# Performance work log

Hardware: AMD Instinct MI355X
Metric: run time of the kernel (lower is better)

The kernel has to match this reference:

```python
import jax, jax.numpy as jnp
import numpy as np

N_MOL = 100000   # molecules in batch
N_ATOMS = 40     # atoms per molecule
R = 2            # resonance representations per molecule


def setup_inputs() -> dict:
    key = jax.random.key(0)
    k1, k2, k3 = jax.random.split(key, 3)
    N = N_MOL * N_ATOMS * R  # flattened atom rows (8M)
    electronegativity = jax.random.normal(k1, (N,), dtype=jnp.float32)
    # hardness must be positive / away from zero (it is inverted)
    hardness = jax.random.uniform(k2, (N,), dtype=jnp.float32, minval=0.5, maxval=1.5)
    formal_charge = jax.random.randint(k3, (N,), -1, 2).astype(jnp.float32)
    idx = jnp.arange(N, dtype=jnp.int32)
    # layout: [mol0 rep0 (40 atoms), mol0 rep1 (40 atoms), mol1 rep0, ...]
    rep_seg = idx // N_ATOMS                       # molecule-representation segment id
    mol = idx // (N_ATOMS * R)
    j = idx % N_ATOMS                              # atom index within molecule
    out_idx = mol * N_ATOMS + j                    # output row for mean over reps
    return {
        "electronegativity": electronegativity,
        "hardness": hardness,
        "formal_charge": formal_charge,
        "rep_seg": rep_seg,
        "out_idx": out_idx,
        "num_segments": N_MOL * R,
        "num_out": N_MOL * N_ATOMS,
        "n_reps": R,
    }


def reference(electronegativity, hardness, formal_charge, rep_seg, out_idx,
              num_segments, num_out, n_reps):
    # Charge equalization (Gilson et al.) per molecule-representation segment s:
    #   inv_h_i = 1/h_i
    #   q_i = inv_h_i * ((dot(inv_h, e) + Q_s) / sum(inv_h) - e_i)
    inv_h = 1.0 / hardness
    A = jax.ops.segment_sum(inv_h, rep_seg, num_segments)                      # sum(1/h)
    B = jax.ops.segment_sum(inv_h * electronegativity, rep_seg, num_segments)  # dot(1/h, e)
    Q = jax.ops.segment_sum(formal_charge, rep_seg, num_segments)              # total charge
    lam = (B + Q) / A                                                          # Lagrange multiplier per segment
    q = inv_h * (lam[rep_seg] - electronegativity)                             # per-atom charge per rep
    # mean over the n_reps representations of each molecule (torch .mean(dim=0) + vstack)
    out = jax.ops.segment_sum(q, out_idx, num_out) / n_reps
    return out.reshape(-1, 1)
```

## Files before the change

kernel.cpp:

```cpp
#include <hip/hip_runtime.h>


typedef float f32x4 __attribute__((ext_vector_type(4)));

#define BLOCK 320
#define MPB   32
#define SEGS  (MPB * 2)

__global__ __launch_bounds__(BLOCK) void cpc_kernel(
    const float* __restrict__ elneg,
    const float* __restrict__ hard,
    const float* __restrict__ fchg,
    float* __restrict__ out,
    int n_mol)
{
    __shared__ float s_pa[SEGS * 11];
    __shared__ float s_pb[SEGS * 11];
    __shared__ float s_pq[SEGS * 11];
    __shared__ float s_lam[SEGS];

    const int t = threadIdx.x;
    const int m = t / 10;
    const int s = t - m * 10;
    const long long mol_base = (long long)blockIdx.x * MPB;
    const int lm = min(MPB, (int)(n_mol - mol_base));
    const bool act = (m < lm);

    const long long g0 = (mol_base + m) * 80 + 4 * s;

    f32x4 h0, e0, f0, h1, e1, f1;
    h0.x=1;h0.y=1;h0.z=1;h0.w=1; h1=h0;
    e0.x=0;e0.y=0;e0.z=0;e0.w=0; e1=e0; f0=e0; f1=e0;
    if (act) {
        h0 = __builtin_nontemporal_load((const f32x4*)(hard  + g0));
        h1 = __builtin_nontemporal_load((const f32x4*)(hard  + g0 + 40));
        e0 = __builtin_nontemporal_load((const f32x4*)(elneg + g0));
        e1 = __builtin_nontemporal_load((const f32x4*)(elneg + g0 + 40));
        f0 = __builtin_nontemporal_load((const f32x4*)(fchg  + g0));
        f1 = __builtin_nontemporal_load((const f32x4*)(fchg  + g0 + 40));
    }

    f32x4 i0, i1;
    i0.x = 1.0f / h0.x; i0.y = 1.0f / h0.y; i0.z = 1.0f / h0.z; i0.w = 1.0f / h0.w;
    i1.x = 1.0f / h1.x; i1.y = 1.0f / h1.y; i1.z = 1.0f / h1.z; i1.w = 1.0f / h1.w;

    if (act) {
        const int b0 = (2 * m)     * 11 + s;
        const int b1 = (2 * m + 1) * 11 + s;
        s_pa[b0] = (i0.x + i0.y) + (i0.z + i0.w);
        s_pb[b0] = (i0.x * e0.x + i0.y * e0.y) + (i0.z * e0.z + i0.w * e0.w);
        s_pq[b0] = (f0.x + f0.y) + (f0.z + f0.w);
        s_pa[b1] = (i1.x + i1.y) + (i1.z + i1.w);
        s_pb[b1] = (i1.x * e1.x + i1.y * e1.y) + (i1.z * e1.z + i1.w * e1.w);
        s_pq[b1] = (f1.x + f1.y) + (f1.z + f1.w);
    }
    __syncthreads();

    if (t < 2 * lm) {
        float A = 0.f, B = 0.f, Q = 0.f;
        #pragma unroll
        for (int k = 0; k < 10; ++k) {
            A += s_pa[t * 11 + k];
            B += s_pb[t * 11 + k];
            Q += s_pq[t * 11 + k];
        }
        s_lam[t] = (B + Q) / A;
    }
    __syncthreads();

    if (act) {
        const float lam0 = s_lam[2 * m];
        const float lam1 = s_lam[2 * m + 1];
        f32x4 o;
        o.x = 0.5f * (i0.x * (lam0 - e0.x) + i1.x * (lam1 - e1.x));
        o.y = 0.5f * (i0.y * (lam0 - e0.y) + i1.y * (lam1 - e1.y));
        o.z = 0.5f * (i0.z * (lam0 - e0.z) + i1.z * (lam1 - e1.z));
        o.w = 0.5f * (i0.w * (lam0 - e0.w) + i1.w * (lam1 - e1.w));
        __builtin_nontemporal_store(o, (f32x4*)(out + (mol_base + m) * 40 + 4 * s));
    }
}

extern "C" void kernel_launch(void* const* d_in, const int* in_sizes, int n_in,
                              void* d_out, int out_size, void* d_ws, size_t ws_size,
                              hipStream_t stream) {
    const float* elneg = (const float*)d_in[0];
    const float* hard  = (const float*)d_in[1];
    const float* fchg  = (const float*)d_in[2];
    float* out = (float*)d_out;

    const int n_mol = out_size / 40;
    const int grid  = (n_mol + MPB - 1) / MPB;
    cpc_kernel<<<grid, BLOCK, 0, stream>>>(elneg, hard, fchg, out, n_mol);
}
```

Measured before the change: 23.93 us.

## Process two chunks per block with prefetch and double-buffered LDS reduction

Each block now handles two 16-molecule chunks. The next chunk's loads are issued before the barrier of the current one, and LDS buffers are double-buffered. Each thread loads one contiguous float4 per array rather than two strided ones, and the per-segment reduction reads vectorized f32x4 partials. Reciprocals use the fast rcp intrinsic, nontemporal loads and stores are dropped, and a launch-bounds occupancy hint is added. This adds LDS traffic for passing the rep-1 values and leaves half the threads idle in the output phase.

```diff
diff --git a/kernel.cpp b/kernel.cpp
--- a/kernel.cpp
+++ b/kernel.cpp
@@ -4,79 +4,103 @@
 typedef float f32x4 __attribute__((ext_vector_type(4)));
 
 #define BLOCK 320
-#define MPB   32
+#define MPB   16
 #define SEGS  (MPB * 2)
+#define PROW  3
 
-__global__ __launch_bounds__(BLOCK) void cpc_kernel(
+static __device__ __forceinline__ float hsum(f32x4 v) {
+    return (v.x + v.y) + (v.z + v.w);
+}
+
+__global__ __launch_bounds__(BLOCK, 8) void cpc_kernel(
     const float* __restrict__ elneg,
     const float* __restrict__ hard,
     const float* __restrict__ fchg,
     float* __restrict__ out,
-    int n_mol)
+    int n_mol, int nchunks)
 {
-    __shared__ float s_pa[SEGS * 11];
-    __shared__ float s_pb[SEGS * 11];
-    __shared__ float s_pq[SEGS * 11];
-    __shared__ float s_lam[SEGS];
+    __shared__ f32x4 s_pa [2][SEGS * PROW];
+    __shared__ f32x4 s_pbq[2][SEGS * PROW];
+    __shared__ f32x4 s_i1 [2][MPB * 10];
+    __shared__ f32x4 s_e1 [2][MPB * 10];
 
-    const int t = threadIdx.x;
-    const int m = t / 10;
-    const int s = t - m * 10;
-    const long long mol_base = (long long)blockIdx.x * MPB;
-    const int lm = min(MPB, (int)(n_mol - mol_base));
-    const bool act = (m < lm);
+    const int t  = threadIdx.x;
+    const int m  = t / 20;
+    const int s2 = t % 20;
+    const int r  = s2 / 10;
+    const int s  = s2 % 10;
 
-    const long long g0 = (mol_base + m) * 80 + 4 * s;
-
-    f32x4 h0, e0, f0, h1, e1, f1;
-    h0.x=1;h0.y=1;h0.z=1;h0.w=1; h1=h0;
-    e0.x=0;e0.y=0;e0.z=0;e0.w=0; e1=e0; f0=e0; f1=e0;
-    if (act) {
-        h0 = __builtin_nontemporal_load((const f32x4*)(hard  + g0));
-        h1 = __builtin_nontemporal_load((const f32x4*)(hard  + g0 + 40));
-        e0 = __builtin_nontemporal_load((const f32x4*)(elneg + g0));
-        e1 = __builtin_nontemporal_load((const f32x4*)(elneg + g0 + 40));
-        f0 = __builtin_nontemporal_load((const f32x4*)(fchg  + g0));
-        f1 = __builtin_nontemporal_load((const f32x4*)(fchg  + g0 + 40));
+    if (t < SEGS) {
+        ((float*)s_pa [0])[t*12+10] = 0.f; ((float*)s_pa [0])[t*12+11] = 0.f;
+        ((float*)s_pa [1])[t*12+10] = 0.f; ((float*)s_pa [1])[t*12+11] = 0.f;
+        ((float*)s_pbq[0])[t*12+10] = 0.f; ((float*)s_pbq[0])[t*12+11] = 0.f;
+        ((float*)s_pbq[1])[t*12+10] = 0.f; ((float*)s_pbq[1])[t*12+11] = 0.f;
     }
 
-    f32x4 i0, i1;
-    i0.x = 1.0f / h0.x; i0.y = 1.0f / h0.y; i0.z = 1.0f / h0.z; i0.w = 1.0f / h0.w;
-    i1.x = 1.0f / h1.x; i1.y = 1.0f / h1.y; i1.z = 1.0f / h1.z; i1.w = 1.0f / h1.w;
+    int c = blockIdx.x * 2;
+    bool act = (c < nchunks) && (c * MPB + m < n_mol);
+    f32x4 hv = {1,1,1,1}, ev = {0,0,0,0}, fv = {0,0,0,0};
+    if (act) {
+        const long long g = (long long)c * (MPB * 80) + 4 * t;
+        hv = *(const f32x4*)(hard  + g);
+        ev = *(const f32x4*)(elneg + g);
+        fv = *(const f32x4*)(fchg  + g);
+    }
 
-    if (act) {
-        const int b0 = (2 * m)     * 11 + s;
-        const int b1 = (2 * m + 1) * 11 + s;
-        s_pa[b0] = (i0.x + i0.y) + (i0.z + i0.w);
-        s_pb[b0] = (i0.x * e0.x + i0.y * e0.y) + (i0.z * e0.z + i0.w * e0.w);
-        s_pq[b0] = (f0.x + f0.y) + (f0.z + f0.w);
-        s_pa[b1] = (i1.x + i1.y) + (i1.z + i1.w);
-        s_pb[b1] = (i1.x * e1.x + i1.y * e1.y) + (i1.z * e1.z + i1.w * e1.w);
-        s_pq[b1] = (f1.x + f1.y) + (f1.z + f1.w);
-    }
-    __syncthreads();
+    int buf = 0;
+    #pragma unroll
+    for (int it = 0; it < 2; ++it) {
+        if (c >= nchunks) break;
 
-    if (t < 2 * lm) {
-        float A = 0.f, B = 0.f, Q = 0.f;
-        #pragma unroll
-        for (int k = 0; k < 10; ++k) {
-            A += s_pa[t * 11 + k];
-            B += s_pb[t * 11 + k];
-            Q += s_pq[t * 11 + k];
+        f32x4 iv;
+        iv.x = __builtin_amdgcn_rcpf(hv.x);
+        iv.y = __builtin_amdgcn_rcpf(hv.y);
+        iv.z = __builtin_amdgcn_rcpf(hv.z);
+        iv.w = __builtin_amdgcn_rcpf(hv.w);
+        const float pa  = hsum(iv);
+        const float pbq = ((iv.x*ev.x + iv.y*ev.y) + (iv.z*ev.z + iv.w*ev.w)) + hsum(fv);
+        if (act) {
+            const int seg = m * 2 + r;
+            ((float*)s_pa [buf])[seg*12 + s] = pa;
+            ((float*)s_pbq[buf])[seg*12 + s] = pbq;
+            if (r) { s_i1[buf][m*10 + s] = iv; s_e1[buf][m*10 + s] = ev; }
         }
-        s_lam[t] = (B + Q) / A;
-    }
-    __syncthreads();
+        const f32x4 i0 = iv, e0 = ev;
+        const int  cc = c;
+        const bool act_cur = act;
 
-    if (act) {
-        const float lam0 = s_lam[2 * m];
-        const float lam1 = s_lam[2 * m + 1];
-        f32x4 o;
-        o.x = 0.5f * (i0.x * (lam0 - e0.x) + i1.x * (lam1 - e1.x));
-        o.y = 0.5f * (i0.y * (lam0 - e0.y) + i1.y * (lam1 - e1.y));
-        o.z = 0.5f * (i0.z * (lam0 - e0.z) + i1.z * (lam1 - e1.z));
-        o.w = 0.5f * (i0.w * (lam0 - e0.w) + i1.w * (lam1 - e1.w));
-        __builtin_nontemporal_store(o, (f32x4*)(out + (mol_base + m) * 40 + 4 * s));
+        c += 1;
+        if (it == 0) {
+            act = (c < nchunks) && (c * MPB + m < n_mol);
+            if (act) {
+                const long long g = (long long)c * (MPB * 80) + 4 * t;
+                hv = *(const f32x4*)(hard  + g);
+                ev = *(const f32x4*)(elneg + g);
+                fv = *(const f32x4*)(fchg  + g);
+            }
+        }
+
+        __syncthreads();
+
+        if (r == 0 && act_cur) {
+            const int row0 = (m*2)     * PROW;
+            const int row1 = (m*2 + 1) * PROW;
+            const float A0 = hsum(s_pa [buf][row0]) + hsum(s_pa [buf][row0+1]) + hsum(s_pa [buf][row0+2]);
+            const float B0 = hsum(s_pbq[buf][row0]) + hsum(s_pbq[buf][row0+1]) + hsum(s_pbq[buf][row0+2]);
+            const float A1 = hsum(s_pa [buf][row1]) + hsum(s_pa [buf][row1+1]) + hsum(s_pa [buf][row1+2]);
+            const float B1 = hsum(s_pbq[buf][row1]) + hsum(s_pbq[buf][row1+1]) + hsum(s_pbq[buf][row1+2]);
+            const float lam0 = B0 / A0;
+            const float lam1 = B1 / A1;
+            const f32x4 i1 = s_i1[buf][m*10 + s];
+            const f32x4 e1 = s_e1[buf][m*10 + s];
+            f32x4 o;
+            o.x = 0.5f * (i0.x * (lam0 - e0.x) + i1.x * (lam1 - e1.x));
+            o.y = 0.5f * (i0.y * (lam0 - e0.y) + i1.y * (lam1 - e1.y));
+            o.z = 0.5f * (i0.z * (lam0 - e0.z) + i1.z * (lam1 - e1.z));
+            o.w = 0.5f * (i0.w * (lam0 - e0.w) + i1.w * (lam1 - e1.w));
+            *(f32x4*)(out + (long long)cc * (MPB * 40) + m * 40 + s * 4) = o;
+        }
+        buf ^= 1;
     }
 }
 
@@ -88,7 +112,8 @@
     const float* fchg  = (const float*)d_in[2];
     float* out = (float*)d_out;
 
-    const int n_mol = out_size / 40;
-    const int grid  = (n_mol + MPB - 1) / MPB;
-    cpc_kernel<<<grid, BLOCK, 0, stream>>>(elneg, hard, fchg, out, n_mol);
+    const int n_mol   = out_size / 40;
+    const int nchunks = (n_mol + MPB - 1) / MPB;
+    const int grid    = (nchunks + 1) / 2;
+    cpc_kernel<<<grid, BLOCK, 0, stream>>>(elneg, hard, fchg, out, n_mol, nchunks);
 }
```

After: 22.79 us. 1.05x faster.
